# Performance work log

Measured on AMD Instinct MI355X. Metric: run time of the kernel, lower is better.

The kernel has to match this reference:

```python
import jax, jax.numpy as jnp
import numpy as np

N, C, T, H, W = 2, 128, 4, 64, 64
NHEAD = 8
HB, WB = 16, 16  # block_size
BNH, BNW = H // HB, W // WB


def setup_inputs() -> dict:
    key = jax.random.key(0)
    ks = jax.random.split(key, 13)
    f = lambda k, sh, s=1.0: jax.random.normal(k, sh, dtype=jnp.float32) * s
    return {
        'q': f(ks[0], (N, C, T, H, W)),
        'k': f(ks[1], (N, C, T, H, W)),
        'v': f(ks[2], (N, C, T, H, W)),
        'pos_q': f(ks[3], (N, C, T, H, W)),
        'pos_k': f(ks[4], (N, C, T, H, W)),
        'w_in_long': f(ks[5], (3 * C, C), 0.05),
        'b_in_long': f(ks[6], (3 * C,), 0.02),
        'w_out_long': f(ks[7], (C, C), 0.05),
        'b_out_long': f(ks[8], (C,), 0.02),
        'w_in_short': f(ks[9], (3 * C, C), 0.05),
        'b_in_short': f(ks[10], (3 * C,), 0.02),
        'w_out_short': f(ks[11], (C, C), 0.05),
        'b_out_short': f(ks[12], (C,), 0.02),
    }


def _mha(q, k, v, w_in, b_in, w_out, b_out):
    # q: (Lq, B, C), k/v: (Lk, B, C); torch nn.MultiheadAttention (eval, no dropout)
    c = q.shape[-1]
    dh = c // NHEAD
    qp = q @ w_in[:c].T + b_in[:c]
    kp = k @ w_in[c:2 * c].T + b_in[c:2 * c]
    vp = v @ w_in[2 * c:].T + b_in[2 * c:]
    Lq, B, _ = qp.shape
    Lk = kp.shape[0]
    qp = qp.reshape(Lq, B, NHEAD, dh) * (1.0 / np.sqrt(dh)).astype(np.float32)
    kp = kp.reshape(Lk, B, NHEAD, dh)
    vp = vp.reshape(Lk, B, NHEAD, dh)
    scores = jnp.einsum('lbhd,mbhd->bhlm', qp, kp)
    attn = jax.nn.softmax(scores, axis=-1)
    out = jnp.einsum('bhlm,mbhd->lbhd', attn, vp).reshape(Lq, B, c)
    return out @ w_out.T + b_out


def _to_long(x, t):
    # (n,c,t,h,w) -> (t*bn_h*bn_w, n*h_b*w_b, c): one pixel per block, attend across blocks
    n, c = x.shape[0], x.shape[1]
    x = x.reshape(n, c, t, BNH, HB, BNW, WB).transpose(2, 3, 5, 0, 4, 6, 1)
    return x.reshape(t * BNH * BNW, n * HB * WB, c)


def _long_to_short(x, t):
    # (t*bn_h*bn_w, n*h_b*w_b, c) -> (t*h_b*w_b, n*bn_h*bn_w, c): attend within block
    c = x.shape[-1]
    x = x.reshape(t, BNH, BNW, -1, HB, WB, c).transpose(0, 4, 5, 3, 1, 2, 6)
    return x.reshape(t * HB * WB, -1, c)


def reference(q, k, v, pos_q, pos_k, w_in_long, b_in_long, w_out_long, b_out_long,
              w_in_short, b_in_short, w_out_short, b_out_short):
    n, c, t_q, h, w = q.shape
    t_k = k.shape[2]
    qb = _to_long(q, t_q)
    kb = _to_long(k, t_k)
    vb = _to_long(v, t_k)
    pqb = _to_long(pos_q, t_q)
    pkb = _to_long(pos_k, t_k)
    # long-range (inter-block) cross attention
    vb = _mha(qb + pqb, kb + pkb, vb, w_in_long, b_in_long, w_out_long, b_out_long)
    vs = _long_to_short(vb, t_q)
    pqs = _long_to_short(pqb, t_q)
    # short-range (intra-block) self attention
    out = _mha(vs + pqs, vs + pqs, vs, w_in_short, b_in_short, w_out_short, b_out_short)
    out = out.reshape(t_q, HB, WB, n, BNH, BNW, c).transpose(3, 6, 0, 4, 1, 5, 2)
    return out.reshape(n, c, t_q, h, w)
```

## Files before the change

kernel.cpp:

```cpp
#include <hip/hip_runtime.h>
#include <hip/hip_bf16.h>

#define CC 128

typedef __attribute__((ext_vector_type(8))) short short8;
typedef __attribute__((ext_vector_type(16))) float f32x16;

union I4S8 { int4 i; short8 s; int2 h[2]; };

__device__ __forceinline__ unsigned short f2bfu(float f) {
  union { float f; unsigned int i; } x; x.f = f;
  unsigned int r = x.i + 0x7fffu + ((x.i >> 16) & 1u);
  return (unsigned short)(r >> 16);
}
__device__ __forceinline__ short f2bfs(float f) { return (short)f2bfu(f); }
__device__ __forceinline__ unsigned int pk2(float a, float b) {
  union { __hip_bfloat162 h; unsigned int u; } c;
  c.h = __float22bfloat162_rn(make_float2(a, b));
  return c.u;
}
__device__ __forceinline__ float bflo(unsigned int u) {
  union { unsigned int i; float f; } x; x.i = u << 16; return x.f;
}
__device__ __forceinline__ float bfhi(unsigned int u) {
  union { unsigned int i; float f; } x; x.i = u & 0xffff0000u; return x.f;
}
__device__ __forceinline__ float exp2_raw(float x) {
#if __has_builtin(__builtin_amdgcn_exp2f)
  return __builtin_amdgcn_exp2f(x);
#else
  return exp2f(x);
#endif
}
__device__ __forceinline__ f32x16 fzero16() {
  f32x16 z;
#pragma unroll
  for (int i = 0; i < 16; ++i) z[i] = 0.f;
  return z;
}
__device__ __forceinline__ void ld16(const float* p, float* f) {
#pragma unroll
  for (int i = 0; i < 4; ++i) {
    float4 a = *(const float4*)(p + 4 * i);
    f[4*i] = a.x; f[4*i+1] = a.y; f[4*i+2] = a.z; f[4*i+3] = a.w;
  }
}

#define QSC 0.3606737602f

__global__ __launch_bounds__(256) void k_cvtw(
    const float* __restrict__ wil, const float* __restrict__ wol,
    const float* __restrict__ wis, const float* __restrict__ wos,
    short* __restrict__ o) {
  const int idx = (blockIdx.x * 256 + threadIdx.x) * 8;
  const float* src; int off;
  if (idx < 49152)       { src = wil; off = idx; }
  else if (idx < 65536)  { src = wol; off = idx - 49152; }
  else if (idx < 114688) { src = wis; off = idx - 65536; }
  else                   { src = wos; off = idx - 114688; }
  float f[8];
  float4 a = *(const float4*)(src + off), b = *(const float4*)(src + off + 4);
  f[0]=a.x; f[1]=a.y; f[2]=a.z; f[3]=a.w; f[4]=b.x; f[5]=b.y; f[6]=b.z; f[7]=b.w;
  short8 r;
#pragma unroll
  for (int j = 0; j < 8; ++j) r[j] = f2bfs(f[j]);
  *(short8*)(o + idx) = r;
}

__global__ __launch_bounds__(256) void k_proj_long(
    const float* __restrict__ q, const float* __restrict__ k,
    const float* __restrict__ v, const float* __restrict__ pq,
    const float* __restrict__ pk,
    const short* __restrict__ wbf, const float* __restrict__ b_in,
    short* __restrict__ qb, short* __restrict__ kb, short* __restrict__ vb,
    short* __restrict__ pos_ct) {
  __shared__ short XQ[32][132], XK[32][132], XV[32][132];
  const int tid = threadIdx.x;
  const int wid = tid >> 6, lane = tid & 63;
  const int l31 = lane & 31, g = lane >> 5;
  const int tok0 = blockIdx.x * 32;
  const int l = tok0 >> 9, b0 = tok0 & 511;
  const int t = l >> 4, bh = (l >> 2) & 3, bw = l & 3;
  const int nb = b0 >> 8, ph0 = (b0 >> 4) & 15;
  {
    const int c = tid >> 1, half = tid & 1;
    const int h = bh * 16 + ph0 + half, w0 = bw * 16;
    const size_t gb = (((size_t)(nb * CC + c) * 4 + t) << 12) + h * 64 + w0;
    float a[16], p[16];
    ld16(q + gb, a); ld16(pq + gb, p);
    {
      short8 s0, s1;
#pragma unroll
      for (int j = 0; j < 8; ++j) { s0[j] = f2bfs(p[j]); s1[j] = f2bfs(p[8 + j]); }
      short* pd = pos_ct + (size_t)c * 32768 + tok0 + half * 16;
      *(short8*)pd = s0;
      *(short8*)(pd + 8) = s1;
    }
#pragma unroll
    for (int j = 0; j < 16; ++j) XQ[half * 16 + j][c] = f2bfs(a[j] + p[j]);
    ld16(k + gb, a); ld16(pk + gb, p);
#pragma unroll
    for (int j = 0; j < 16; ++j) XK[half * 16 + j][c] = f2bfs(a[j] + p[j]);
    ld16(v + gb, a);
#pragma unroll
    for (int j = 0; j < 16; ++j) XV[half * 16 + j][c] = f2bfs(a[j]);
  }
  __syncthreads();
  for (int i = 0; i < 3; ++i) {
    const int nt = wid + 4 * i;
    const int nch = nt * 32 + l31;
    const int which = nt >> 2;
    const short (*X)[132] = (which == 0) ? XQ : (which == 1) ? XK : XV;
    f32x16 acc = fzero16();
#pragma unroll
    for (int k0 = 0; k0 < 128; k0 += 16) {
      I4S8 af;
      af.h[0] = *(const int2*)&X[l31][k0 + 8 * g];
      af.h[1] = *(const int2*)&X[l31][k0 + 8 * g + 4];
      short8 bf = *(const short8*)(wbf + nch * CC + k0 + 8 * g);
      acc = __builtin_amdgcn_mfma_f32_32x32x16_bf16(af.s, bf, acc, 0, 0, 0);
    }
    const float bias = b_in[nch];
    const int hh = (nch >> 4) & 7, d = nch & 15;
    short* dst = (which == 0) ? qb : (which == 1) ? kb : vb;
    const float sc = (which == 0) ? QSC : 1.0f;
#pragma unroll
    for (int r = 0; r < 16; ++r) {
      const int tt = (r & 3) + 8 * (r >> 2) + 4 * g;
      dst[((size_t)((b0 + tt) * 8 + hh) * 64 + l) * 16 + d] =
          f2bfs((acc[r] + bias) * sc);
    }
  }
}

template<int SEQ, int BATCH>
__global__ __launch_bounds__(256) void k_attn(
    const short* __restrict__ qsp, const short* __restrict__ ksp,
    const short* __restrict__ vsp, short* __restrict__ ao) {
  __shared__ short vt[4][17 * 36];
  const int tid = threadIdx.x;
  const int wid = tid >> 6, lane = tid & 63;
  const int l31 = lane & 31, g = lane >> 5;
  const int WPP = SEQ / 32;
  const int blk = ((blockIdx.x & 7) << 8) | (blockIdx.x >> 3);
  const int gw = blk * 4 + wid;
  const int pair = gw / WPP;
  const int q0 = (gw % WPP) * 32;
  const int batch = pair >> 3, hh = pair & 7;
  const size_t pbase = (size_t)pair * (SEQ * 16);
  short* vtw = &vt[wid][0];
  if (lane < 18) *(int*)(vtw + 16 * 36 + 2 * lane) = 0x3F803F80;

  const short8 qf = *(const short8*)(qsp + pbase + (size_t)(q0 + l31) * 16 + 8 * g);

  f32x16 acc = fzero16();
  const int arow = (l31 < 16) ? l31 : 16;
  const short* vtr = vtw + arow * 36;

  for (int k0 = 0; k0 < SEQ; k0 += 32) {
    const short8 kf = *(const short8*)(ksp + pbase + (size_t)(k0 + l31) * 16 + 8 * g);
    const short8 vf = *(const short8*)(vsp + pbase + (size_t)(k0 + l31) * 16 + 8 * g);
#pragma unroll
    for (int j = 0; j < 8; ++j)
      vtw[(8 * g + j) * 36 + l31] = vf[j];

    f32x16 s = __builtin_amdgcn_mfma_f32_32x32x16_bf16(kf, qf, fzero16(), 0, 0, 0);

    I4S8 pa, pb;
#pragma unroll
    for (int j = 0; j < 4; ++j) {
      pa.i[j] = (int)pk2(exp2_raw(s[2 * j]), exp2_raw(s[2 * j + 1]));
      pb.i[j] = (int)pk2(exp2_raw(s[8 + 2 * j]), exp2_raw(s[9 + 2 * j]));
    }

    I4S8 a1, a2;
    a1.h[0] = *(const int2*)(vtr + 4 * g);
    a1.h[1] = *(const int2*)(vtr + 8 + 4 * g);
    a2.h[0] = *(const int2*)(vtr + 16 + 4 * g);
    a2.h[1] = *(const int2*)(vtr + 24 + 4 * g);
    acc = __builtin_amdgcn_mfma_f32_32x32x16_bf16(a1.s, pa.s, acc, 0, 0, 0);
    acc = __builtin_amdgcn_mfma_f32_32x32x16_bf16(a2.s, pb.s, acc, 0, 0, 0);
  }

  const float inv = 1.0f / acc[8];
  const int qi = q0 + l31;
  short* dst = ao + ((size_t)qi * BATCH + batch) * CC + hh * 16 + 4 * g;
  uint2 o1, o2;
  o1.x = pk2(acc[0] * inv, acc[1] * inv);
  o1.y = pk2(acc[2] * inv, acc[3] * inv);
  o2.x = pk2(acc[4] * inv, acc[5] * inv);
  o2.y = pk2(acc[6] * inv, acc[7] * inv);
  *(uint2*)dst = o1;
  *(uint2*)(dst + 8) = o2;
}

__global__ __launch_bounds__(256) void k_mid(
    const short* __restrict__ ao, const short* __restrict__ pos_ct,
    const short* __restrict__ wobf, const float* __restrict__ b_out_l,
    const short* __restrict__ wibf, const float* __restrict__ b_in_s,
    short* __restrict__ qb, short* __restrict__ kb, short* __restrict__ vb) {
  __shared__ short YQK[32][132], YV[32][132];
  const int tid = threadIdx.x;
  const int wid = tid >> 6, lane = tid & 63;
  const int l31 = lane & 31, g = lane >> 5;
  const int tok0 = blockIdx.x * 32;
  const int l = tok0 >> 9, b0 = tok0 & 511;
  const int t = l >> 4, bh = (l >> 2) & 3, bw = l & 3;
  const int nb = b0 >> 8, ph0 = (b0 >> 4) & 15;
  {
    const int nch = wid * 32 + l31;
    f32x16 acc = fzero16();
#pragma unroll
    for (int k0 = 0; k0 < 128; k0 += 16) {
      short8 af = *(const short8*)(ao + (size_t)(tok0 + l31) * CC + k0 + 8 * g);
      short8 bf = *(const short8*)(wobf + nch * CC + k0 + 8 * g);
      acc = __builtin_amdgcn_mfma_f32_32x32x16_bf16(af, bf, acc, 0, 0, 0);
    }
    const float bias = b_out_l[nch];
    float pos[16];
#pragma unroll
    for (int rr = 0; rr < 4; ++rr) {
      int2 pp = *(const int2*)(pos_ct + (size_t)nch * 32768 + tok0 + rr * 8 + 4 * g);
      pos[rr * 4 + 0] = bflo((unsigned int)pp.x);
      pos[rr * 4 + 1] = bfhi((unsigned int)pp.x);
      pos[rr * 4 + 2] = bflo((unsigned int)pp.y);
      pos[rr * 4 + 3] = bfhi((unsigned int)pp.y);
    }
#pragma unroll
    for (int r = 0; r < 16; ++r) {
      const int tt = (r & 3) + 8 * (r >> 2) + 4 * g;
      const float y = acc[r] + bias;
      YV[tt][nch] = f2bfs(y);
      YQK[tt][nch] = f2bfs(y + pos[r]);
    }
  }
  __syncthreads();
  const int bs = nb * 16 + bh * 4 + bw;
  const int ls0 = (t * 16 + ph0) * 16;
  for (int i = 0; i < 3; ++i) {
    const int nt = wid + 4 * i;
    const int nch = nt * 32 + l31;
    const int which = nt >> 2;
    const short (*X)[132] = (which == 2) ? YV : YQK;
    f32x16 acc = fzero16();
#pragma unroll
    for (int k0 = 0; k0 < 128; k0 += 16) {
      I4S8 af;
      af.h[0] = *(const int2*)&X[l31][k0 + 8 * g];
      af.h[1] = *(const int2*)&X[l31][k0 + 8 * g + 4];
      short8 bf = *(const short8*)(wibf + nch * CC + k0 + 8 * g);
      acc = __builtin_amdgcn_mfma_f32_32x32x16_bf16(af.s, bf, acc, 0, 0, 0);
    }
    const float bias = b_in_s[nch];
    const int hh = (nch >> 4) & 7, d = nch & 15;
    short* dst = (which == 0) ? qb : (which == 1) ? kb : vb;
    const float sc = (which == 0) ? QSC : 1.0f;
    const size_t base = ((size_t)(bs * 8 + hh) * 1024 + ls0) * 16 + d;
#pragma unroll
    for (int r = 0; r < 16; ++r) {
      const int tt = (r & 3) + 8 * (r >> 2) + 4 * g;
      dst[base + (size_t)tt * 16] = f2bfs((acc[r] + bias) * sc);
    }
  }
}

__global__ __launch_bounds__(256) void k_out_short(
    const short* __restrict__ ao, const short* __restrict__ wbf,
    const float* __restrict__ b_out, float* __restrict__ out) {
  const int tid = threadIdx.x;
  const int wid = tid >> 6, lane = tid & 63;
  const int l31 = lane & 31, g = lane >> 5;
  const int bs = blockIdx.x & 31;
  const int qi0 = (blockIdx.x >> 5) << 5;
  const int nb = bs >> 4, bh = (bs >> 2) & 3, bw = bs & 3;
  const int t = qi0 >> 8, ph0 = (qi0 >> 4) & 15;
  const int nch = wid * 32 + l31;
  f32x16 acc = fzero16();
#pragma unroll
  for (int k0 = 0; k0 < 128; k0 += 16) {
    short8 af = *(const short8*)(ao + ((size_t)(qi0 + l31) * 32 + bs) * CC + k0 + 8 * g);
    short8 bf = *(const short8*)(wbf + nch * CC + k0 + 8 * g);
    acc = __builtin_amdgcn_mfma_f32_32x32x16_bf16(af, bf, acc, 0, 0, 0);
  }
  const float bias = b_out[nch];
#pragma unroll
  for (int rr = 0; rr < 4; ++rr) {
    const int tt0 = rr * 8 + 4 * g;
    const int ph_off = tt0 >> 4, pw = tt0 & 15;
    const int h = bh * 16 + ph0 + ph_off, w = bw * 16 + pw;
    const size_t adr = (((size_t)(nb * CC + nch) * 4 + t) << 12) + h * 64 + w;
    float4 f;
    f.x = acc[rr * 4 + 0] + bias; f.y = acc[rr * 4 + 1] + bias;
    f.z = acc[rr * 4 + 2] + bias; f.w = acc[rr * 4 + 3] + bias;
    *(float4*)(out + adr) = f;
  }
}

extern "C" void kernel_launch(void* const* d_in, const int* in_sizes, int n_in,
                              void* d_out, int out_size, void* d_ws, size_t ws_size,
                              hipStream_t stream) {
  (void)in_sizes; (void)n_in; (void)out_size; (void)ws_size;
  const float* q   = (const float*)d_in[0];
  const float* k   = (const float*)d_in[1];
  const float* v   = (const float*)d_in[2];
  const float* pq  = (const float*)d_in[3];
  const float* pk  = (const float*)d_in[4];
  const float* wil = (const float*)d_in[5];
  const float* bil = (const float*)d_in[6];
  const float* wol = (const float*)d_in[7];
  const float* bol = (const float*)d_in[8];
  const float* wis = (const float*)d_in[9];
  const float* bis = (const float*)d_in[10];
  const float* wos = (const float*)d_in[11];
  const float* bos = (const float*)d_in[12];

  short* qs     = (short*)d_ws;
  short* ksb    = qs + 4194304;
  short* vsb    = ksb + 4194304;
  short* ao     = vsb + 4194304;
  short* pos_ct = ao + 4194304;
  short* wbf    = pos_ct + 4194304;

  k_cvtw<<<dim3(64), dim3(256), 0, stream>>>(wil, wol, wis, wos, wbf);
  k_proj_long<<<dim3(1024), dim3(256), 0, stream>>>(q, k, v, pq, pk, wbf, bil,
                                                    qs, ksb, vsb, pos_ct);
  k_attn<64, 512><<<dim3(2048), dim3(256), 0, stream>>>(qs, ksb, vsb, ao);
  k_mid<<<dim3(1024), dim3(256), 0, stream>>>(ao, pos_ct, wbf + 49152, bol,
                                              wbf + 65536, bis, qs, ksb, vsb);
  k_attn<1024, 32><<<dim3(2048), dim3(256), 0, stream>>>(qs, ksb, vsb, ao);
  k_out_short<<<dim3(1024), dim3(256), 0, stream>>>(ao, wbf + 114688, bos,
                                                    (float*)d_out);
}
```

Baseline: 150.0 us.

## Pre-transpose V into per-tile global layout with ones row, drop LDS transpose

```diff
diff --git a/kernel.cpp b/kernel.cpp
--- a/kernel.cpp
+++ b/kernel.cpp
@@ -47,6 +47,7 @@
 }
 
 #define QSC 0.3606737602f
+#define VTILE 544
 
 __global__ __launch_bounds__(256) void k_cvtw(
     const float* __restrict__ wil, const float* __restrict__ wol,
@@ -72,7 +73,7 @@
     const float* __restrict__ v, const float* __restrict__ pq,
     const float* __restrict__ pk,
     const short* __restrict__ wbf, const float* __restrict__ b_in,
-    short* __restrict__ qb, short* __restrict__ kb, short* __restrict__ vb,
+    short* __restrict__ qb, short* __restrict__ kb, short* __restrict__ vt,
     short* __restrict__ pos_ct) {
   __shared__ short XQ[32][132], XK[32][132], XV[32][132];
   const int tid = threadIdx.x;
@@ -122,13 +123,24 @@
     }
     const float bias = b_in[nch];
     const int hh = (nch >> 4) & 7, d = nch & 15;
-    short* dst = (which == 0) ? qb : (which == 1) ? kb : vb;
-    const float sc = (which == 0) ? QSC : 1.0f;
-#pragma unroll
-    for (int r = 0; r < 16; ++r) {
-      const int tt = (r & 3) + 8 * (r >> 2) + 4 * g;
-      dst[((size_t)((b0 + tt) * 8 + hh) * 64 + l) * 16 + d] =
-          f2bfs((acc[r] + bias) * sc);
+    if (which == 2) {
+      const int kt = l >> 5, col = l & 31;
+#pragma unroll
+      for (int r = 0; r < 16; ++r) {
+        const int tt = (r & 3) + 8 * (r >> 2) + 4 * g;
+        const size_t pb_ = ((size_t)((b0 + tt) * 8 + hh) * 2 + kt) * VTILE;
+        vt[pb_ + d * 32 + col] = f2bfs(acc[r] + bias);
+        if (d == 0) vt[pb_ + 16 * 32 + col] = (short)0x3F80;
+      }
+    } else {
+      short* dst = (which == 0) ? qb : kb;
+      const float sc = (which == 0) ? QSC : 1.0f;
+#pragma unroll
+      for (int r = 0; r < 16; ++r) {
+        const int tt = (r & 3) + 8 * (r >> 2) + 4 * g;
+        dst[((size_t)((b0 + tt) * 8 + hh) * 64 + l) * 16 + d] =
+            f2bfs((acc[r] + bias) * sc);
+      }
     }
   }
 }
@@ -136,34 +148,28 @@
 template<int SEQ, int BATCH>
 __global__ __launch_bounds__(256) void k_attn(
     const short* __restrict__ qsp, const short* __restrict__ ksp,
-    const short* __restrict__ vsp, short* __restrict__ ao) {
-  __shared__ short vt[4][17 * 36];
+    const short* __restrict__ vt, short* __restrict__ ao) {
   const int tid = threadIdx.x;
   const int wid = tid >> 6, lane = tid & 63;
   const int l31 = lane & 31, g = lane >> 5;
-  const int WPP = SEQ / 32;
+  const int WPP = SEQ / 32, NT = SEQ / 32;
   const int blk = ((blockIdx.x & 7) << 8) | (blockIdx.x >> 3);
   const int gw = blk * 4 + wid;
   const int pair = gw / WPP;
   const int q0 = (gw % WPP) * 32;
   const int batch = pair >> 3, hh = pair & 7;
   const size_t pbase = (size_t)pair * (SEQ * 16);
-  short* vtw = &vt[wid][0];
-  if (lane < 18) *(int*)(vtw + 16 * 36 + 2 * lane) = 0x3F803F80;
+  const int arow = (l31 < 16) ? l31 : 16;
+  const short* vtp = vt + (size_t)pair * (NT * VTILE) + arow * 32;
 
   const short8 qf = *(const short8*)(qsp + pbase + (size_t)(q0 + l31) * 16 + 8 * g);
 
   f32x16 acc = fzero16();
-  const int arow = (l31 < 16) ? l31 : 16;
-  const short* vtr = vtw + arow * 36;
-
-  for (int k0 = 0; k0 < SEQ; k0 += 32) {
-    const short8 kf = *(const short8*)(ksp + pbase + (size_t)(k0 + l31) * 16 + 8 * g);
-    const short8 vf = *(const short8*)(vsp + pbase + (size_t)(k0 + l31) * 16 + 8 * g);
-#pragma unroll
-    for (int j = 0; j < 8; ++j)
-      vtw[(8 * g + j) * 36 + l31] = vf[j];
-
+
+#pragma unroll 2
+  for (int kt = 0; kt < NT; ++kt) {
+    const short8 kf =
+        *(const short8*)(ksp + pbase + (size_t)(kt * 32 + l31) * 16 + 8 * g);
     f32x16 s = __builtin_amdgcn_mfma_f32_32x32x16_bf16(kf, qf, fzero16(), 0, 0, 0);
 
     I4S8 pa, pb;
@@ -173,11 +179,12 @@
       pb.i[j] = (int)pk2(exp2_raw(s[8 + 2 * j]), exp2_raw(s[9 + 2 * j]));
     }
 
+    const short* vtt = vtp + kt * VTILE;
     I4S8 a1, a2;
-    a1.h[0] = *(const int2*)(vtr + 4 * g);
-    a1.h[1] = *(const int2*)(vtr + 8 + 4 * g);
-    a2.h[0] = *(const int2*)(vtr + 16 + 4 * g);
-    a2.h[1] = *(const int2*)(vtr + 24 + 4 * g);
+    a1.h[0] = *(const int2*)(vtt + 4 * g);
+    a1.h[1] = *(const int2*)(vtt + 8 + 4 * g);
+    a2.h[0] = *(const int2*)(vtt + 16 + 4 * g);
+    a2.h[1] = *(const int2*)(vtt + 24 + 4 * g);
     acc = __builtin_amdgcn_mfma_f32_32x32x16_bf16(a1.s, pa.s, acc, 0, 0, 0);
     acc = __builtin_amdgcn_mfma_f32_32x32x16_bf16(a2.s, pb.s, acc, 0, 0, 0);
   }
@@ -198,7 +205,7 @@
     const short* __restrict__ ao, const short* __restrict__ pos_ct,
     const short* __restrict__ wobf, const float* __restrict__ b_out_l,
     const short* __restrict__ wibf, const float* __restrict__ b_in_s,
-    short* __restrict__ qb, short* __restrict__ kb, short* __restrict__ vb) {
+    short* __restrict__ qb, short* __restrict__ kb, short* __restrict__ vt) {
   __shared__ short YQK[32][132], YV[32][132];
   const int tid = threadIdx.x;
   const int wid = tid >> 6, lane = tid & 63;
@@ -253,13 +260,30 @@
     }
     const float bias = b_in_s[nch];
     const int hh = (nch >> 4) & 7, d = nch & 15;
-    short* dst = (which == 0) ? qb : (which == 1) ? kb : vb;
-    const float sc = (which == 0) ? QSC : 1.0f;
-    const size_t base = ((size_t)(bs * 8 + hh) * 1024 + ls0) * 16 + d;
-#pragma unroll
-    for (int r = 0; r < 16; ++r) {
-      const int tt = (r & 3) + 8 * (r >> 2) + 4 * g;
-      dst[base + (size_t)tt * 16] = f2bfs((acc[r] + bias) * sc);
+    if (which == 2) {
+      const int kt = ls0 >> 5;
+      const size_t base2 = ((size_t)(bs * 8 + hh) * 32 + kt) * VTILE;
+#pragma unroll
+      for (int rr = 0; rr < 4; ++rr) {
+        const int c0 = rr * 8 + 4 * g;
+        uint2 wv;
+        wv.x = pk2(acc[rr * 4 + 0] + bias, acc[rr * 4 + 1] + bias);
+        wv.y = pk2(acc[rr * 4 + 2] + bias, acc[rr * 4 + 3] + bias);
+        *(uint2*)(vt + base2 + d * 32 + c0) = wv;
+        if (d == 0) {
+          uint2 on; on.x = 0x3F803F80u; on.y = 0x3F803F80u;
+          *(uint2*)(vt + base2 + 16 * 32 + c0) = on;
+        }
+      }
+    } else {
+      short* dst = (which == 0) ? qb : kb;
+      const float sc = (which == 0) ? QSC : 1.0f;
+      const size_t base = ((size_t)(bs * 8 + hh) * 1024 + ls0) * 16 + d;
+#pragma unroll
+      for (int r = 0; r < 16; ++r) {
+        const int tt = (r & 3) + 8 * (r >> 2) + 4 * g;
+        dst[base + (size_t)tt * 16] = f2bfs((acc[r] + bias) * sc);
+      }
     }
   }
 }
@@ -316,18 +340,18 @@
 
   short* qs     = (short*)d_ws;
   short* ksb    = qs + 4194304;
-  short* vsb    = ksb + 4194304;
-  short* ao     = vsb + 4194304;
+  short* ao     = ksb + 4194304;
   short* pos_ct = ao + 4194304;
   short* wbf    = pos_ct + 4194304;
+  short* vt     = wbf + 131072;
 
   k_cvtw<<<dim3(64), dim3(256), 0, stream>>>(wil, wol, wis, wos, wbf);
   k_proj_long<<<dim3(1024), dim3(256), 0, stream>>>(q, k, v, pq, pk, wbf, bil,
-                                                    qs, ksb, vsb, pos_ct);
-  k_attn<64, 512><<<dim3(2048), dim3(256), 0, stream>>>(qs, ksb, vsb, ao);
+                                                    qs, ksb, vt, pos_ct);
+  k_attn<64, 512><<<dim3(2048), dim3(256), 0, stream>>>(qs, ksb, vt, ao);
   k_mid<<<dim3(1024), dim3(256), 0, stream>>>(ao, pos_ct, wbf + 49152, bol,
-                                              wbf + 65536, bis, qs, ksb, vsb);
-  k_attn<1024, 32><<<dim3(2048), dim3(256), 0, stream>>>(qs, ksb, vsb, ao);
+                                              wbf + 65536, bis, qs, ksb, vt);
+  k_attn<1024, 32><<<dim3(2048), dim3(256), 0, stream>>>(qs, ksb, vt, ao);
   k_out_short<<<dim3(1024), dim3(256), 0, stream>>>(ao, wbf + 114688, bos,
                                                     (float*)d_out);
 }
```

Result: slower. 160.5 us (+7.0%).
